# Kernel optimization log

Hardware: AMD Instinct MI355X
Metric: run time of the kernel (lower is better)

The kernel has to match this reference:

```python
import jax, jax.numpy as jnp
import numpy as np

# Static problem dims (match input_specs / init_kwargs)
B, NQ, C, H = 2, 900, 256, 8
HGT, WID = 64, 64            # single-scale feature map (input_spatial_shapes = [[64, 64]])
N = HGT * WID                # 4096 keys
DH = C // H                  # head dim 32
RPE_HID = 512
STRIDE = 16                  # feature_stride


def setup_inputs() -> dict:
    key = jax.random.key(0)
    ks = jax.random.split(key, 24)
    p = lambda k, shape: jax.random.normal(k, shape, jnp.float32) * 0.02
    # reference boxes (cx, cy, w, h) in pixel coords of a 1024x1024 image
    ref = jax.random.uniform(ks[0], (B, NQ, 1, 4), jnp.float32)
    ref = jnp.concatenate([ref[..., :2] * (WID * STRIDE), ref[..., 2:] * 128.0], axis=-1)
    return {
        "vggt_features": jnp.zeros((1,), jnp.float32),  # unused by forward (kept for signature fidelity)
        "query": jax.random.normal(ks[1], (B, NQ, C), jnp.float32),
        "reference_2d": ref,
        "k_input_flatten": jax.random.normal(ks[2], (B, N, C), jnp.float32),
        "v_input_flatten": jax.random.normal(ks[3], (B, N, C), jnp.float32),
        "input_spatial_shapes": jnp.array([[HGT, WID]], jnp.int32),
        "input_padding_mask": jnp.zeros((B, N), jnp.bool_),
        # cpb_mlp1 (x) and cpb_mlp2 (y): Linear(2,512)+ReLU+Linear(512,H,no bias); stored as [in,out]
        "W1x": p(ks[4], (2, RPE_HID)), "b1x": jnp.zeros((RPE_HID,), jnp.float32), "W2x": p(ks[5], (RPE_HID, H)),
        "W1y": p(ks[6], (2, RPE_HID)), "b1y": jnp.zeros((RPE_HID,), jnp.float32), "W2y": p(ks[7], (RPE_HID, H)),
        "Wq": p(ks[8], (C, C)), "bq": jnp.zeros((C,), jnp.float32),
        "Wk": p(ks[9], (C, C)), "bk": jnp.zeros((C,), jnp.float32),
        "Wv": p(ks[10], (C, C)), "bv": jnp.zeros((C,), jnp.float32),
        "Wp": p(ks[11], (C, C)), "bp": jnp.zeros((C,), jnp.float32),
    }


def _mlp(d, W1, b1, W2):
    return jax.nn.relu(d @ W1 + b1) @ W2


def reference(vggt_features, query, reference_2d, k_input_flatten, v_input_flatten,
              input_spatial_shapes, input_padding_mask,
              W1x, b1x, W2x, W1y, b1y, W2y, Wq, bq, Wk, bk, Wv, bv, Wp, bp):
    h, w = HGT, WID  # static (input_spatial_shapes[0] == [HGT, WID])
    scale = DH ** -0.5
    # cxcywh -> xyxy: [B, NQ, 1, 4]
    xyxy = jnp.concatenate([reference_2d[..., :2] - reference_2d[..., 2:] / 2,
                            reference_2d[..., :2] + reference_2d[..., 2:] / 2], axis=-1)
    # pixel-center grid coords (linspace(0.5, w-0.5, w) * stride)
    pos_x = ((jnp.arange(w, dtype=jnp.float32) + 0.5) * STRIDE)[None, None, :, None]
    pos_y = ((jnp.arange(h, dtype=jnp.float32) + 0.5) * STRIDE)[None, None, :, None]
    delta_x = xyxy[..., 0::2] - pos_x  # [B, NQ, w, 2]  (x1, x2 rel. to columns)
    delta_y = xyxy[..., 1::2] - pos_y  # [B, NQ, h, 2]  (y1, y2 rel. to rows)
    rpe_x = _mlp(delta_x, W1x, b1x, W2x)  # [B, NQ, w, H]
    rpe_y = _mlp(delta_y, W1y, b1y, W2y)  # [B, NQ, h, H]
    # broadcast add over (row, col) then flatten spatial -> [B, H, NQ, N]
    rpe = (rpe_x[:, :, None] + rpe_y[:, :, :, None]).reshape(B, NQ, h * w, H).transpose(0, 3, 1, 2)
    q = (query @ Wq + bq).reshape(B, NQ, H, DH).transpose(0, 2, 1, 3) * scale  # [B,H,NQ,DH]
    k = (k_input_flatten @ Wk + bk).reshape(B, N, H, DH).transpose(0, 2, 1, 3)  # [B,H,N,DH]
    v = (v_input_flatten @ Wv + bv).reshape(B, N, H, DH).transpose(0, 2, 1, 3)  # [B,H,N,DH]
    attn = jnp.einsum('bhqd,bhkd->bhqk', q, k) + rpe
    attn = attn + input_padding_mask[:, None, None, :].astype(attn.dtype) * (-100.0)
    # torch.clip_ to finfo(min,max) is an identity on finite values; softmax follows
    attn = jax.nn.softmax(attn, axis=-1)
    x = jnp.einsum('bhqk,bhkd->bhqd', attn, v).transpose(0, 2, 1, 3).reshape(B, NQ, C)
    return x @ Wp + bp
```

## Files before the change

kernel.cpp:

```cpp
#include <hip/hip_runtime.h>
#include <hip/hip_bf16.h>
#include <cmath>

#define B_ 2
#define NQ_ 900
#define N_ 4096
#define LOG2E 1.4426950408889634f

typedef __attribute__((ext_vector_type(4))) float f32x4;
typedef __attribute__((ext_vector_type(8))) short s16x8;
typedef __attribute__((ext_vector_type(8))) _Float16 f16x8;

__device__ inline short f2bf(float x) {
    union { __hip_bfloat16 b; short s; } u;
    u.b = __float2bfloat16(x);
    return u.s;
}
__device__ inline short f2h(float x) {
    _Float16 h = (_Float16)x;
    return __builtin_bit_cast(short, h);
}

template <int CTRL>
__device__ inline float dppf(float x) {
    int xi = __builtin_bit_cast(int, x);
    int r = __builtin_amdgcn_update_dpp(xi, xi, CTRL, 0xF, 0xF, true);
    return __builtin_bit_cast(float, r);
}
__device__ inline float rowmax16(float v) {
    v = fmaxf(v, dppf<0x121>(v));
    v = fmaxf(v, dppf<0x122>(v));
    v = fmaxf(v, dppf<0x124>(v));
    v = fmaxf(v, dppf<0x128>(v));
    return v;
}
__device__ inline float rowsum16(float v) {
    v += dppf<0x121>(v);
    v += dppf<0x122>(v);
    v += dppf<0x124>(v);
    v += dppf<0x128>(v);
    return v;
}

__global__ __launch_bounds__(256) void proj_kernel(
    const float* __restrict__ query, const float* __restrict__ kin,
    const float* __restrict__ vin,
    const float* __restrict__ Wq, const float* __restrict__ Wk,
    const float* __restrict__ Wv,
    const float* __restrict__ bqv, const float* __restrict__ bkv,
    const float* __restrict__ bvv,
    unsigned short* __restrict__ qbf, unsigned short* __restrict__ kbf,
    unsigned short* __restrict__ vbf, float qscale)
{
    const int mtx = blockIdx.z;
    const float* X = mtx == 0 ? query : mtx == 1 ? kin : vin;
    const float* W = mtx == 0 ? Wq : mtx == 1 ? Wk : Wv;
    const float* bias = mtx == 0 ? bqv : mtx == 1 ? bkv : bvv;
    unsigned short* Y = mtx == 0 ? qbf : mtx == 1 ? kbf : vbf;
    const int M = mtx == 0 ? 1800 : 8192;
    const int m0 = blockIdx.x * 64;
    if (m0 >= M) return;
    const float alpha = mtx == 0 ? qscale : 1.0f;
    const int rows_per_b = mtx == 0 ? 900 : 4096;
    const int ROWS = mtx == 0 ? 960 : 4096;

    __shared__ short Ab[16384];
    __shared__ short Bb[16384];
    const int tid = threadIdx.x;
    const int w = tid >> 6, l = tid & 63, quad = l >> 4, l15 = l & 15;
    const int wq = tid & 3, mm = tid >> 2;

    {
        const bool valid = (m0 + mm) < M;
        const float* xr = X + (size_t)(m0 + mm) * 256;
        #pragma unroll
        for (int it = 0; it < 8; ++it) {
            int g2 = it * 4 + wq;
            float4 a0 = make_float4(0.f, 0.f, 0.f, 0.f), a1 = a0;
            if (valid) {
                a0 = *(const float4*)(xr + g2 * 8);
                a1 = *(const float4*)(xr + g2 * 8 + 4);
            }
            uint4 pk;
            pk.x = (unsigned)(unsigned short)f2bf(a0.x) | ((unsigned)(unsigned short)f2bf(a0.y) << 16);
            pk.y = (unsigned)(unsigned short)f2bf(a0.z) | ((unsigned)(unsigned short)f2bf(a0.w) << 16);
            pk.z = (unsigned)(unsigned short)f2bf(a1.x) | ((unsigned)(unsigned short)f2bf(a1.y) << 16);
            pk.w = (unsigned)(unsigned short)f2bf(a1.z) | ((unsigned)(unsigned short)f2bf(a1.w) << 16);
            *(uint4*)(Ab + (it * 256 + mm * 4 + wq) * 8) = pk;
        }
    }

    for (int nt0 = 0; nt0 < 4; ++nt0) {
        const int n0 = nt0 * 64;
        {
            const float* wcol = W + n0 + mm;
            #pragma unroll
            for (int it = 0; it < 8; ++it) {
                int g2 = it * 4 + wq;
                uint4 wk4;
                wk4.x = (unsigned)(unsigned short)f2bf(wcol[(g2 * 8 + 0) * 256])
                      | ((unsigned)(unsigned short)f2bf(wcol[(g2 * 8 + 1) * 256]) << 16);
                wk4.y = (unsigned)(unsigned short)f2bf(wcol[(g2 * 8 + 2) * 256])
                      | ((unsigned)(unsigned short)f2bf(wcol[(g2 * 8 + 3) * 256]) << 16);
                wk4.z = (unsigned)(unsigned short)f2bf(wcol[(g2 * 8 + 4) * 256])
                      | ((unsigned)(unsigned short)f2bf(wcol[(g2 * 8 + 5) * 256]) << 16);
                wk4.w = (unsigned)(unsigned short)f2bf(wcol[(g2 * 8 + 6) * 256])
                      | ((unsigned)(unsigned short)f2bf(wcol[(g2 * 8 + 7) * 256]) << 16);
                *(uint4*)(Bb + (it * 256 + mm * 4 + wq) * 8) = wk4;
            }
        }
        __syncthreads();

        f32x4 acc[4] = {{0.f,0.f,0.f,0.f},{0.f,0.f,0.f,0.f},{0.f,0.f,0.f,0.f},{0.f,0.f,0.f,0.f}};
        #pragma unroll
        for (int kc = 0; kc < 8; ++kc) {
            s16x8 a = *(const s16x8*)(Ab + (kc * 256 + (w * 16 + l15) * 4 + quad) * 8);
            #pragma unroll
            for (int nt = 0; nt < 4; ++nt) {
                s16x8 bf = *(const s16x8*)(Bb + (kc * 256 + (nt * 16 + l15) * 4 + quad) * 8);
                acc[nt] = __builtin_amdgcn_mfma_f32_16x16x32_bf16(a, bf, acc[nt], 0, 0, 0);
            }
        }
        __syncthreads();

        #pragma unroll
        for (int nt = 0; nt < 4; ++nt) {
            int n = n0 + nt * 16 + l15;
            float bs = bias[n];
            int h = n >> 5, d = n & 31;
            #pragma unroll
            for (int r = 0; r < 4; ++r) {
                int row = m0 + w * 16 + quad * 4 + r;
                if (row < M) {
                    int b = row / rows_per_b;
                    int pos = row - b * rows_per_b;
                    Y[((size_t)(b * 8 + h) * ROWS + pos) * 32 + d] =
                        (unsigned short)f2bf((acc[nt][r] + bs) * alpha);
                }
            }
        }
    }
}

__global__ __launch_bounds__(256) void outproj_kernel(
    const float* __restrict__ X, const float* __restrict__ W,
    const float* __restrict__ bias, float* __restrict__ Y, int M)
{
    __shared__ short Abh[4096], Abl[4096], Bbh[4096], Bbl[4096];
    const int tid = threadIdx.x;
    const int m0 = blockIdx.x * 64, n0 = blockIdx.y * 64;
    const int w = tid >> 6, l = tid & 63, quad = l >> 4, l15 = l & 15;
    const int wq = tid & 3, mm = tid >> 2;
    const bool valid = (m0 + mm) < M;
    const float* xr = X + (size_t)(m0 + mm) * 256;
    const float* wcol = W + n0 + mm;

    f32x4 acc[4] = {{0.f,0.f,0.f,0.f},{0.f,0.f,0.f,0.f},{0.f,0.f,0.f,0.f},{0.f,0.f,0.f,0.f}};

    for (int kq = 0; kq < 4; ++kq) {
        #pragma unroll
        for (int it = 0; it < 2; ++it) {
            int g2 = it * 4 + wq;
            int kbase = kq * 64 + g2 * 8;
            float av[8], bv[8];
            #pragma unroll
            for (int j = 0; j < 8; ++j) {
                av[j] = valid ? xr[kbase + j] : 0.f;
                bv[j] = wcol[(kbase + j) * 256];
            }
            uint4 ah, al, bh, bl;
            unsigned* ahp = (unsigned*)&ah; unsigned* alp = (unsigned*)&al;
            unsigned* bhp = (unsigned*)&bh; unsigned* blp = (unsigned*)&bl;
            #pragma unroll
            for (int j2 = 0; j2 < 4; ++j2) {
                _Float16 h0 = (_Float16)av[j2 * 2], h1 = (_Float16)av[j2 * 2 + 1];
                ahp[j2] = (unsigned)(unsigned short)__builtin_bit_cast(short, h0)
                        | ((unsigned)(unsigned short)__builtin_bit_cast(short, h1) << 16);
                alp[j2] = (unsigned)(unsigned short)f2h(av[j2 * 2] - (float)h0)
                        | ((unsigned)(unsigned short)f2h(av[j2 * 2 + 1] - (float)h1) << 16);
                _Float16 g0 = (_Float16)bv[j2 * 2], g1 = (_Float16)bv[j2 * 2 + 1];
                bhp[j2] = (unsigned)(unsigned short)__builtin_bit_cast(short, g0)
                        | ((unsigned)(unsigned short)__builtin_bit_cast(short, g1) << 16);
                blp[j2] = (unsigned)(unsigned short)f2h(bv[j2 * 2] - (float)g0)
                        | ((unsigned)(unsigned short)f2h(bv[j2 * 2 + 1] - (float)g1) << 16);
            }
            int gi = (it * 256 + mm * 4 + wq) * 8;
            *(uint4*)(Abh + gi) = ah;
            *(uint4*)(Abl + gi) = al;
            *(uint4*)(Bbh + gi) = bh;
            *(uint4*)(Bbl + gi) = bl;
        }
        __syncthreads();

        #pragma unroll
        for (int kc = 0; kc < 2; ++kc) {
            int ga = (kc * 256 + (w * 16 + l15) * 4 + quad) * 8;
            f16x8 ah = *(const f16x8*)(Abh + ga);
            f16x8 al = *(const f16x8*)(Abl + ga);
            #pragma unroll
            for (int nt = 0; nt < 4; ++nt) {
                int gb = (kc * 256 + (nt * 16 + l15) * 4 + quad) * 8;
                f16x8 bh = *(const f16x8*)(Bbh + gb);
                f16x8 bl = *(const f16x8*)(Bbl + gb);
                acc[nt] = __builtin_amdgcn_mfma_f32_16x16x32_f16(ah, bh, acc[nt], 0, 0, 0);
                acc[nt] = __builtin_amdgcn_mfma_f32_16x16x32_f16(ah, bl, acc[nt], 0, 0, 0);
                acc[nt] = __builtin_amdgcn_mfma_f32_16x16x32_f16(al, bh, acc[nt], 0, 0, 0);
            }
        }
        __syncthreads();
    }

    #pragma unroll
    for (int nt = 0; nt < 4; ++nt) {
        int n = n0 + nt * 16 + l15;
        float bs = bias[n];
        #pragma unroll
        for (int r = 0; r < 4; ++r) {
            int row = m0 + w * 16 + quad * 4 + r;
            if (row < M)
                Y[(size_t)row * 256 + n] = acc[nt][r] + bs;
        }
    }
}

__global__ __launch_bounds__(512) void rpe3_kernel(
    const float* __restrict__ ref2d,
    const float* __restrict__ W1x, const float* __restrict__ b1x,
    const float* __restrict__ W1y, const float* __restrict__ b1y,
    const float* __restrict__ W2x, const float* __restrict__ W2y,
    float* __restrict__ rpe_x, float* __restrict__ rpe_y)
{
    __shared__ short sw2h[8192], sw2l[8192];
    __shared__ float4 sUV[2 * 576];

    const int tid = threadIdx.x;
    for (int i = tid; i < 8192; i += 512) {
        int g = i >> 3, j = i & 7;
        int kcg = g >> 6, rr = g & 63, n = rr >> 2, q4 = rr & 3;
        int k = kcg * 32 + q4 * 8 + j;
        float val = ((n < 8) ? W2x[k * 8 + n] : W2y[k * 8 + (n - 8)]) * LOG2E;
        _Float16 hi = (_Float16)val;
        sw2h[i] = __builtin_bit_cast(short, hi);
        sw2l[i] = f2h(val - (float)hi);
    }
    {
        int k = tid;
        float w1x0 = W1x[k], w1x1 = W1x[512 + k];
        float w1y0 = W1y[k], w1y1 = W1y[512 + k];
        float bx = b1x[k], by = b1y[k];
        float vx = -(w1x0 + w1x1), vy = -(w1y0 + w1y1);
        #pragma unroll
        for (int q2 = 0; q2 < 2; ++q2) {
            const float4 bb = *(const float4*)(ref2d + (size_t)(blockIdx.x * 2 + q2) * 4);
            float ux = fmaf(w1x0, bb.x - bb.z * 0.5f, fmaf(w1x1, bb.x + bb.z * 0.5f, bx));
            float uy = fmaf(w1y0, bb.y - bb.w * 0.5f, fmaf(w1y1, bb.y + bb.w * 0.5f, by));
            sUV[q2 * 576 + (k >> 3) * 9 + (k & 7)] = make_float4(ux, vx, uy, vy);
        }
    }

    const int w = tid >> 6, l = tid & 63, quad = l >> 4, l15 = l & 15;
    const int qi = w >> 2, wrow = w & 3;
    const int bq = blockIdx.x * 2 + qi;
    const int row = wrow * 16 + l15;
    const float pc = (row + 0.5f) * 16.0f;

    __syncthreads();

    f32x4 accx = {0.f, 0.f, 0.f, 0.f}, accy = {0.f, 0.f, 0.f, 0.f};
    for (int kc = 0; kc < 16; ++kc) {
        f16x8 axh, axl, ayh, ayl;
        #pragma unroll
        for (int i = 0; i < 8; ++i) {
            float4 u = sUV[qi * 576 + (kc * 4 + quad) * 9 + i];
            float hx = fmaxf(fmaf(u.y, pc, u.x), 0.f);
            float hy = fmaxf(fmaf(u.w, pc, u.z), 0.f);
            _Float16 xh = (_Float16)hx;
            _Float16 yh = (_Float16)hy;
            axh[i] = xh;
            axl[i] = (_Float16)(hx - (float)xh);
            ayh[i] = yh;
            ayl[i] = (_Float16)(hy - (float)yh);
        }
        f16x8 bh = *(const f16x8*)(sw2h + (kc * 64 + l15 * 4 + quad) * 8);
        f16x8 bl = *(const f16x8*)(sw2l + (kc * 64 + l15 * 4 + quad) * 8);
        accx = __builtin_amdgcn_mfma_f32_16x16x32_f16(axh, bh, accx, 0, 0, 0);
        accx = __builtin_amdgcn_mfma_f32_16x16x32_f16(axh, bl, accx, 0, 0, 0);
        accx = __builtin_amdgcn_mfma_f32_16x16x32_f16(axl, bh, accx, 0, 0, 0);
        accy = __builtin_amdgcn_mfma_f32_16x16x32_f16(ayh, bh, accy, 0, 0, 0);
        accy = __builtin_amdgcn_mfma_f32_16x16x32_f16(ayh, bl, accy, 0, 0, 0);
        accy = __builtin_amdgcn_mfma_f32_16x16x32_f16(ayl, bh, accy, 0, 0, 0);
    }

    #pragma unroll
    for (int rr = 0; rr < 4; ++rr) {
        int row_out = wrow * 16 + quad * 4 + rr;
        if (l15 < 8) rpe_x[((size_t)l15 * 1800 + bq) * 64 + row_out] = accx[rr];
        else         rpe_y[((size_t)(l15 - 8) * 1800 + bq) * 64 + row_out] = accy[rr];
    }
}

__global__ __launch_bounds__(512, 4) void attn_mfma_kernel(
    const unsigned short* __restrict__ qb16, const unsigned short* __restrict__ kb16,
    const unsigned short* __restrict__ vb16,
    const float* __restrict__ rpe_x, const float* __restrict__ rpe_y,
    const unsigned char* __restrict__ mask, float* __restrict__ xout)
{
    __shared__ short skf[4 * 2048];
    __shared__ short svt[4 * 2048];
    __shared__ short spb[8 * 544];
    __shared__ float ry[32 * 65];
    __shared__ unsigned long long smaskb[64];
    __shared__ float sm[8][16], sl[8][16], sLf[32];

    const int tid = threadIdx.x;
    const int qb = blockIdx.x, h = blockIdx.y, b = blockIdx.z;
    const int q0 = qb * 32;
    const int w = tid >> 6, l = tid & 63;
    const int qsub = w >> 2, g = w & 3;
    const int quad = l >> 4, l15 = l & 15;

    const unsigned short* qg = qb16 + (size_t)(b * 8 + h) * 960 * 32;
    const unsigned short* kg = kb16 + (size_t)(b * 8 + h) * 4096 * 32;
    const unsigned short* vg = vb16 + (size_t)(b * 8 + h) * 4096 * 32;
    const float* rxh = rpe_x + ((size_t)h * 1800 + b * NQ_) * 64;
    const float* ryh = rpe_y + ((size_t)h * 1800 + b * NQ_) * 64;

    for (int i = tid; i < 2048; i += 512) {
        int qq = q0 + (i >> 6), pos = i & 63;
        float vy = 0.f;
        if (qq < NQ_)
            vy = ryh[(size_t)qq * 64 + pos];
        ry[(i >> 6) * 65 + pos] = vy;
    }
    #pragma unroll
    for (int j = 0; j < 8; ++j) {
        int c = w * 8 + j;
        unsigned long long bits = __ballot(mask[(size_t)b * N_ + c * 64 + l] != 0);
        if (l == 0) smaskb[c] = bits;
    }

    s16x8 qa = *(const s16x8*)(qg + (size_t)(q0 + qsub * 16 + l15) * 32 + quad * 8);

    f32x4 rx4[4];
    #pragma unroll
    for (int t = 0; t < 4; ++t)
        #pragma unroll
        for (int r = 0; r < 4; ++r) {
            int qq = q0 + qsub * 16 + quad * 4 + r;
            rx4[t][r] = (qq < NQ_) ? rxh[(size_t)qq * 64 + t * 16 + l15] : 0.f;
        }

    const int sg = tid >> 7, role = (tid >> 6) & 1, stl = tid & 63;
    int eoff[4];
    if (role == 0) {
        #pragma unroll
        for (int t = 0; t < 4; ++t)
            eoff[t] = (t * 16 + (stl & 15)) * 32 + (stl >> 4) * 8;
    } else {
        #pragma unroll
        for (int t = 0; t < 4; ++t)
            eoff[t] = stl * 32 + t * 8;
    }
    const unsigned short* src = role ? vg : kg;

    uint4 pf[4];
    {
        size_t cb = (size_t)(sg * 16) * 2048;
        #pragma unroll
        for (int t = 0; t < 4; ++t) pf[t] = *(const uint4*)(src + cb + eoff[t]);
    }

    float mrow[4] = {-INFINITY, -INFINITY, -INFINITY, -INFINITY};
    float lrow[4] = {0.f, 0.f, 0.f, 0.f};
    f32x4 acc0 = {0.f, 0.f, 0.f, 0.f}, acc1 = {0.f, 0.f, 0.f, 0.f};
    short* pw = spb + w * 544;

    for (int i = 0; i < 16; ++i) {
        __syncthreads();
        if (role == 0) {
            #pragma unroll
            for (int t = 0; t < 4; ++t)
                *(uint4*)(skf + sg * 2048 + (t * 64 + stl) * 8) = pf[t];
        } else {
            short* vtw = svt + sg * 2048;
            #pragma unroll
            for (int t = 0; t < 4; ++t) {
                const unsigned short* pv = (const unsigned short*)&pf[t];
                #pragma unroll
                for (int j = 0; j < 8; ++j) {
                    int d = t * 8 + j;
                    vtw[d * 64 + (((stl >> 3) ^ (d & 7)) << 3) + (stl & 7)] = (short)pv[j];
                }
            }
        }
        __syncthreads();

        {
            int inext = (i + 1 < 16) ? i + 1 : 15;
            size_t cb = (size_t)(sg * 16 + inext) * 2048;
            #pragma unroll
            for (int t = 0; t < 4; ++t) pf[t] = *(const uint4*)(src + cb + eoff[t]);
        }

        const int cgc = g * 16 + i;
        const short* kf = skf + g * 2048;

        f32x4 sc[4];
        #pragma unroll
        for (int t = 0; t < 4; ++t) {
            s16x8 kb = *(const s16x8*)(kf + (t * 64 + l) * 8);
            sc[t] = __builtin_amdgcn_mfma_f32_16x16x32_bf16(qa, kb, rx4[t], 0, 0, 0);
        }
        float ryv[4];
        #pragma unroll
        for (int r = 0; r < 4; ++r)
            ryv[r] = ry[(qsub * 16 + quad * 4 + r) * 65 + cgc];
        unsigned long long mb = smaskb[cgc];
        if (mb) {
            #pragma unroll
            for (int t = 0; t < 4; ++t) {
                float mk = ((mb >> (t * 16 + l15)) & 1ULL) ? -144.2695f : 0.f;
                #pragma unroll
                for (int r = 0; r < 4; ++r) sc[t][r] += mk;
            }
        }

        float cmr[4];
        #pragma unroll
        for (int r = 0; r < 4; ++r)
            cmr[r] = fmaxf(fmaxf(sc[0][r], sc[1][r]), fmaxf(sc[2][r], sc[3][r])) + ryv[r];

        int ok = (cmr[0] <= mrow[0] + 8.f) & (cmr[1] <= mrow[1] + 8.f)
               & (cmr[2] <= mrow[2] + 8.f) & (cmr[3] <= mrow[3] + 8.f);
        if (!__all(ok)) {
            #pragma unroll
            for (int r = 0; r < 4; ++r) {
                float cm = rowmax16(cmr[r]);
                float mnew = fmaxf(mrow[r], cm);
                float al = exp2f(mrow[r] - mnew);
                mrow[r] = mnew;
                lrow[r] *= al;
                acc0[r] *= al;
                acc1[r] *= al;
            }
        }

        float msub[4];
        #pragma unroll
        for (int r = 0; r < 4; ++r) msub[r] = mrow[r] - ryv[r];
        #pragma unroll
        for (int t = 0; t < 4; ++t)
            #pragma unroll
            for (int r = 0; r < 4; ++r)
                sc[t][r] = exp2f(sc[t][r] - msub[r]);
        #pragma unroll
        for (int r = 0; r < 4; ++r)
            lrow[r] += (sc[0][r] + sc[1][r]) + (sc[2][r] + sc[3][r]);

        const short* vt = svt + g * 2048;
        #pragma unroll
        for (int hh = 0; hh < 2; ++hh) {
            #pragma unroll
            for (int tt = 0; tt < 2; ++tt) {
                int t = hh * 2 + tt;
                int gphys = (tt * 2 + (l15 >> 3)) ^ quad;
                #pragma unroll
                for (int r = 0; r < 4; ++r)
                    pw[(gphys * 17 + quad * 4 + r) * 8 + (l15 & 7)] = f2bf(sc[t][r]);
            }
            int gph_r = quad ^ (l15 >> 2);
            s16x8 pa  = *(const s16x8*)(pw + (gph_r * 17 + l15) * 8);
            int ksw = ((hh * 4 + quad) ^ (l15 & 7)) * 8;
            s16x8 vb0 = *(const s16x8*)(vt + l15 * 64 + ksw);
            s16x8 vb1 = *(const s16x8*)(vt + (16 + l15) * 64 + ksw);
            acc0 = __builtin_amdgcn_mfma_f32_16x16x32_bf16(pa, vb0, acc0, 0, 0, 0);
            acc1 = __builtin_amdgcn_mfma_f32_16x16x32_bf16(pa, vb1, acc1, 0, 0, 0);
        }
    }

    #pragma unroll
    for (int r = 0; r < 4; ++r) lrow[r] = rowsum16(lrow[r]);

    __syncthreads();
    if (l15 == 0) {
        #pragma unroll
        for (int r = 0; r < 4; ++r) {
            sm[w][quad * 4 + r] = mrow[r];
            sl[w][quad * 4 + r] = lrow[r];
        }
    }
    __syncthreads();
    float wgt[4], L4[4];
    #pragma unroll
    for (int r = 0; r < 4; ++r) {
        int qrow = quad * 4 + r;
        float mm = -INFINITY;
        #pragma unroll
        for (int gg = 0; gg < 4; ++gg) mm = fmaxf(mm, sm[qsub * 4 + gg][qrow]);
        float LL = 0.f;
        #pragma unroll
        for (int gg = 0; gg < 4; ++gg)
            LL += exp2f(sm[qsub * 4 + gg][qrow] - mm) * sl[qsub * 4 + gg][qrow];
        wgt[r] = exp2f(mrow[r] - mm);
        L4[r] = LL;
    }
    if (g == 0 && l15 == 0) {
        #pragma unroll
        for (int r = 0; r < 4; ++r) sLf[qsub * 16 + quad * 4 + r] = L4[r];
    }

    float* obuf = (float*)skf;
    for (int gg = 0; gg < 4; ++gg) {
        if (g == gg) {
            #pragma unroll
            for (int r = 0; r < 4; ++r) {
                int idx = (qsub * 16 + quad * 4 + r) * 33 + l15;
                float v0 = wgt[r] * acc0[r];
                float v1 = wgt[r] * acc1[r];
                if (gg == 0) { obuf[idx] = v0; obuf[idx + 16] = v1; }
                else         { obuf[idx] += v0; obuf[idx + 16] += v1; }
            }
        }
        __syncthreads();
    }

    for (int i = tid; i < 1024; i += 512) {
        int ql = i >> 5, d = i & 31;
        int qq = q0 + ql;
        if (qq < NQ_)
            xout[(size_t)(b * NQ_ + qq) * 256 + h * 32 + d] = obuf[ql * 33 + d] / sLf[ql];
    }
}

extern "C" void kernel_launch(void* const* d_in, const int* in_sizes, int n_in,
                              void* d_out, int out_size, void* d_ws, size_t ws_size,
                              hipStream_t stream)
{
    const float* query = (const float*)d_in[1];
    const float* ref2d = (const float*)d_in[2];
    const float* kin   = (const float*)d_in[3];
    const float* vin   = (const float*)d_in[4];
    const unsigned char* mask = (const unsigned char*)d_in[6];
    const float* W1x = (const float*)d_in[7];
    const float* b1x = (const float*)d_in[8];
    const float* W2x = (const float*)d_in[9];
    const float* W1y = (const float*)d_in[10];
    const float* b1y = (const float*)d_in[11];
    const float* W2y = (const float*)d_in[12];
    const float* Wq  = (const float*)d_in[13];
    const float* bq  = (const float*)d_in[14];
    const float* Wk  = (const float*)d_in[15];
    const float* bk  = (const float*)d_in[16];
    const float* Wv  = (const float*)d_in[17];
    const float* bv  = (const float*)d_in[18];
    const float* Wp  = (const float*)d_in[19];
    const float* bp  = (const float*)d_in[20];

    char* wsb = (char*)d_ws;
    unsigned short* qbf = (unsigned short*)(wsb);
    unsigned short* kbf = (unsigned short*)(wsb +   983040);
    unsigned short* vbf = (unsigned short*)(wsb +  5177344);
    float* rxws = (float*)(wsb +  9371648);
    float* ryws = (float*)(wsb + 13058048);
    float* xws  = (float*)(wsb + 16744448);
    float* out  = (float*)d_out;

    const float qscale = LOG2E / sqrtf(32.0f);

    proj_kernel<<<dim3(128, 1, 3), 256, 0, stream>>>(
        query, kin, vin, Wq, Wk, Wv, bq, bk, bv, qbf, kbf, vbf, qscale);
    rpe3_kernel<<<900, 512, 0, stream>>>(
        ref2d, W1x, b1x, W1y, b1y, W2x, W2y, rxws, ryws);
    attn_mfma_kernel<<<dim3(29, 8, B_), 512, 0, stream>>>(
        qbf, kbf, vbf, rxws, ryws, mask, xws);
    outproj_kernel<<<dim3(29, 4), 256, 0, stream>>>(xws, Wp, bp, out, 1800);
}
```

Before: 232.6 us.

## Split attention keys across two blocks and merge partial softmax results

Splits the 4096 keys into two halves handled by separate workgroups (split-K flash-decoding style), doubling the attention grid from 464 to 928 blocks so more of the GPU's compute units stay busy. Each block writes unnormalized partial outputs plus row max and sum to workspace. A new merge kernel rescales and combines the two partials into the final per-head output. This adds an extra kernel launch and extra workspace traffic in exchange for better occupancy.

```diff
diff --git a/kernel.cpp b/kernel.cpp
--- a/kernel.cpp
+++ b/kernel.cpp
@@ -303,50 +303,52 @@
     const unsigned short* __restrict__ qb16, const unsigned short* __restrict__ kb16,
     const unsigned short* __restrict__ vb16,
     const float* __restrict__ rpe_x, const float* __restrict__ rpe_y,
-    const unsigned char* __restrict__ mask, float* __restrict__ xout)
+    const unsigned char* __restrict__ mask, float* __restrict__ part)
 {
     __shared__ short skf[4 * 2048];
     __shared__ short svt[4 * 2048];
     __shared__ short spb[8 * 544];
-    __shared__ float ry[32 * 65];
-    __shared__ unsigned long long smaskb[64];
-    __shared__ float sm[8][16], sl[8][16], sLf[32];
+    __shared__ float sry[32 * 33];
+    __shared__ unsigned long long smaskb[32];
+    __shared__ float sm[8][16], sl[8][16], sMf[32], sLf[32];
 
     const int tid = threadIdx.x;
-    const int qb = blockIdx.x, h = blockIdx.y, b = blockIdx.z;
+    const int qb = blockIdx.x, b = blockIdx.z;
+    const int h = blockIdx.y & 7, kv = blockIdx.y >> 3;
     const int q0 = qb * 32;
     const int w = tid >> 6, l = tid & 63;
-    const int qsub = w >> 2, g = w & 3;
+    const int qsub = w >> 3 ? 0 : 0;
+    const int qs = w >> 2, g = w & 3;
     const int quad = l >> 4, l15 = l & 15;
 
     const unsigned short* qg = qb16 + (size_t)(b * 8 + h) * 960 * 32;
-    const unsigned short* kg = kb16 + (size_t)(b * 8 + h) * 4096 * 32;
-    const unsigned short* vg = vb16 + (size_t)(b * 8 + h) * 4096 * 32;
+    const unsigned short* kg = kb16 + (size_t)(b * 8 + h) * 4096 * 32 + (size_t)kv * 2048 * 32;
+    const unsigned short* vg = vb16 + (size_t)(b * 8 + h) * 4096 * 32 + (size_t)kv * 2048 * 32;
     const float* rxh = rpe_x + ((size_t)h * 1800 + b * NQ_) * 64;
     const float* ryh = rpe_y + ((size_t)h * 1800 + b * NQ_) * 64;
 
-    for (int i = tid; i < 2048; i += 512) {
-        int qq = q0 + (i >> 6), pos = i & 63;
+    for (int i = tid; i < 1024; i += 512) {
+        int qq = q0 + (i >> 5), p = i & 31;
         float vy = 0.f;
         if (qq < NQ_)
-            vy = ryh[(size_t)qq * 64 + pos];
-        ry[(i >> 6) * 65 + pos] = vy;
+            vy = ryh[(size_t)qq * 64 + kv * 32 + p];
+        sry[(i >> 5) * 33 + p] = vy;
     }
     #pragma unroll
-    for (int j = 0; j < 8; ++j) {
-        int c = w * 8 + j;
-        unsigned long long bits = __ballot(mask[(size_t)b * N_ + c * 64 + l] != 0);
+    for (int j = 0; j < 4; ++j) {
+        int c = w * 4 + j;
+        unsigned long long bits = __ballot(mask[(size_t)b * N_ + (kv * 32 + c) * 64 + l] != 0);
         if (l == 0) smaskb[c] = bits;
     }
 
-    s16x8 qa = *(const s16x8*)(qg + (size_t)(q0 + qsub * 16 + l15) * 32 + quad * 8);
+    s16x8 qa = *(const s16x8*)(qg + (size_t)(q0 + qs * 16 + l15) * 32 + quad * 8);
 
     f32x4 rx4[4];
     #pragma unroll
     for (int t = 0; t < 4; ++t)
         #pragma unroll
         for (int r = 0; r < 4; ++r) {
-            int qq = q0 + qsub * 16 + quad * 4 + r;
+            int qq = q0 + qs * 16 + quad * 4 + r;
             rx4[t][r] = (qq < NQ_) ? rxh[(size_t)qq * 64 + t * 16 + l15] : 0.f;
         }
 
@@ -365,7 +367,7 @@
 
     uint4 pf[4];
     {
-        size_t cb = (size_t)(sg * 16) * 2048;
+        size_t cb = (size_t)(sg * 8) * 2048;
         #pragma unroll
         for (int t = 0; t < 4; ++t) pf[t] = *(const uint4*)(src + cb + eoff[t]);
     }
@@ -375,7 +377,7 @@
     f32x4 acc0 = {0.f, 0.f, 0.f, 0.f}, acc1 = {0.f, 0.f, 0.f, 0.f};
     short* pw = spb + w * 544;
 
-    for (int i = 0; i < 16; ++i) {
+    for (int i = 0; i < 8; ++i) {
         __syncthreads();
         if (role == 0) {
             #pragma unroll
@@ -396,13 +398,13 @@
         __syncthreads();
 
         {
-            int inext = (i + 1 < 16) ? i + 1 : 15;
-            size_t cb = (size_t)(sg * 16 + inext) * 2048;
+            int inext = (i + 1 < 8) ? i + 1 : 7;
+            size_t cb = (size_t)(sg * 8 + inext) * 2048;
             #pragma unroll
             for (int t = 0; t < 4; ++t) pf[t] = *(const uint4*)(src + cb + eoff[t]);
         }
 
-        const int cgc = g * 16 + i;
+        const int lc = g * 8 + i;
         const short* kf = skf + g * 2048;
 
         f32x4 sc[4];
@@ -414,8 +416,8 @@
         float ryv[4];
         #pragma unroll
         for (int r = 0; r < 4; ++r)
-            ryv[r] = ry[(qsub * 16 + quad * 4 + r) * 65 + cgc];
-        unsigned long long mb = smaskb[cgc];
+            ryv[r] = sry[(qs * 16 + quad * 4 + r) * 33 + lc];
+        unsigned long long mb = smaskb[lc];
         if (mb) {
             #pragma unroll
             for (int t = 0; t < 4; ++t) {
@@ -490,23 +492,27 @@
         }
     }
     __syncthreads();
-    float wgt[4], L4[4];
+    float wgt[4], L4[4], M4[4];
     #pragma unroll
     for (int r = 0; r < 4; ++r) {
         int qrow = quad * 4 + r;
         float mm = -INFINITY;
         #pragma unroll
-        for (int gg = 0; gg < 4; ++gg) mm = fmaxf(mm, sm[qsub * 4 + gg][qrow]);
+        for (int gg = 0; gg < 4; ++gg) mm = fmaxf(mm, sm[qs * 4 + gg][qrow]);
         float LL = 0.f;
         #pragma unroll
         for (int gg = 0; gg < 4; ++gg)
-            LL += exp2f(sm[qsub * 4 + gg][qrow] - mm) * sl[qsub * 4 + gg][qrow];
+            LL += exp2f(sm[qs * 4 + gg][qrow] - mm) * sl[qs * 4 + gg][qrow];
         wgt[r] = exp2f(mrow[r] - mm);
         L4[r] = LL;
+        M4[r] = mm;
     }
     if (g == 0 && l15 == 0) {
         #pragma unroll
-        for (int r = 0; r < 4; ++r) sLf[qsub * 16 + quad * 4 + r] = L4[r];
+        for (int r = 0; r < 4; ++r) {
+            sLf[qs * 16 + quad * 4 + r] = L4[r];
+            sMf[qs * 16 + quad * 4 + r] = M4[r];
+        }
     }
 
     float* obuf = (float*)skf;
@@ -514,7 +520,7 @@
         if (g == gg) {
             #pragma unroll
             for (int r = 0; r < 4; ++r) {
-                int idx = (qsub * 16 + quad * 4 + r) * 33 + l15;
+                int idx = (qs * 16 + quad * 4 + r) * 33 + l15;
                 float v0 = wgt[r] * acc0[r];
                 float v1 = wgt[r] * acc1[r];
                 if (gg == 0) { obuf[idx] = v0; obuf[idx + 16] = v1; }
@@ -524,11 +530,43 @@
         __syncthreads();
     }
 
-    for (int i = tid; i < 1024; i += 512) {
-        int ql = i >> 5, d = i & 31;
-        int qq = q0 + ql;
-        if (qq < NQ_)
-            xout[(size_t)(b * NQ_ + qq) * 256 + h * 32 + d] = obuf[ql * 33 + d] / sLf[ql];
+    float* po = part + (size_t)(((b * 8 + h) * 29 + qb) * 2 + kv) * 1088;
+    for (int i = tid; i < 1024; i += 512)
+        po[i] = obuf[(i >> 5) * 33 + (i & 31)];
+    if (tid < 32) {
+        po[1024 + tid] = sMf[tid];
+        po[1056 + tid] = sLf[tid];
+    }
+}
+
+__global__ __launch_bounds__(256) void attn_merge_kernel(
+    const float* __restrict__ part, float* __restrict__ xout)
+{
+    const int qb = blockIdx.x, h = blockIdx.y, b = blockIdx.z;
+    const float* p0 = part + (size_t)(((b * 8 + h) * 29 + qb) * 2) * 1088;
+    const float* p1 = p0 + 1088;
+    __shared__ float a0s[32], a1s[32], iLs[32];
+    const int tid = threadIdx.x;
+    if (tid < 32) {
+        float m0 = p0[1024 + tid], m1 = p1[1024 + tid];
+        float M = fmaxf(m0, m1);
+        float a0 = exp2f(m0 - M), a1 = exp2f(m1 - M);
+        float L = a0 * p0[1056 + tid] + a1 * p1[1056 + tid];
+        a0s[tid] = a0; a1s[tid] = a1; iLs[tid] = 1.0f / L;
+    }
+    __syncthreads();
+    int i = tid * 4;
+    int ql = i >> 5, d = i & 31;
+    int qq = qb * 32 + ql;
+    if (qq < NQ_) {
+        const f32x4 v0 = *(const f32x4*)(p0 + i);
+        const f32x4 v1 = *(const f32x4*)(p1 + i);
+        float a0 = a0s[ql], a1 = a1s[ql], iL = iLs[ql];
+        f32x4 o;
+        #pragma unroll
+        for (int j = 0; j < 4; ++j)
+            o[j] = (a0 * v0[j] + a1 * v1[j]) * iL;
+        *(f32x4*)(&xout[(size_t)(b * NQ_ + qq) * 256 + h * 32 + d]) = o;
     }
 }
 
@@ -563,6 +601,7 @@
     float* rxws = (float*)(wsb +  9371648);
     float* ryws = (float*)(wsb + 13058048);
     float* xws  = (float*)(wsb + 16744448);
+    float* part = (float*)(wsb + 18587648);
     float* out  = (float*)d_out;
 
     const float qscale = LOG2E / sqrtf(32.0f);
@@ -571,7 +610,8 @@
         query, kin, vin, Wq, Wk, Wv, bq, bk, bv, qbf, kbf, vbf, qscale);
     rpe3_kernel<<<900, 512, 0, stream>>>(
         ref2d, W1x, b1x, W1y, b1y, W2x, W2y, rxws, ryws);
-    attn_mfma_kernel<<<dim3(29, 8, B_), 512, 0, stream>>>(
-        qbf, kbf, vbf, rxws, ryws, mask, xws);
+    attn_mfma_kernel<<<dim3(29, 16, B_), 512, 0, stream>>>(
+        qbf, kbf, vbf, rxws, ryws, mask, part);
+    attn_merge_kernel<<<dim3(29, 8, B_), 256, 0, stream>>>(part, xws);
     outproj_kernel<<<dim3(29, 4), 256, 0, stream>>>(xws, Wp, bp, out, 1800);
 }
```

New measurement: 235.0 us. No clear change (+1.0%).

## Pre-convert and transpose weights once in a prep kernel, read B operands from global

Applied to the files above, without the earlier changes.

Adds a prep kernel that converts Wq/Wk/Wv to bf16, Wp to fp16 hi/lo pairs, and W2x/W2y to scaled fp16 hi/lo, all in transposed layouts. The projection, output-projection and RPE kernels then load B operands directly from global or L2 instead of each block redoing strided fp32 loads and conversions into shared memory. This removes redundant per-block weight conversion and shared memory use. It adds a kernel launch, and the MFMA loops now wait on global loads rather than LDS reads.

```diff
diff --git a/kernel.cpp b/kernel.cpp
--- a/kernel.cpp
+++ b/kernel.cpp
@@ -42,11 +42,75 @@
     return v;
 }
 
+__global__ __launch_bounds__(256) void prep_kernel(
+    const float* __restrict__ Wq, const float* __restrict__ Wk,
+    const float* __restrict__ Wv, const float* __restrict__ Wp,
+    const float* __restrict__ W2x, const float* __restrict__ W2y,
+    unsigned short* __restrict__ wtq, unsigned short* __restrict__ wtk,
+    unsigned short* __restrict__ wtv, unsigned short* __restrict__ wph,
+    unsigned short* __restrict__ wpl, unsigned short* __restrict__ w2h,
+    unsigned short* __restrict__ w2l)
+{
+    const int bx = blockIdx.x;
+    const int tid = threadIdx.x;
+    if (bx == 64) {
+        for (int i = tid; i < 8192; i += 256) {
+            int g = i >> 3, j = i & 7;
+            int kcg = g >> 6, rr = g & 63, n = rr >> 2, q4 = rr & 3;
+            int k = kcg * 32 + q4 * 8 + j;
+            float val = ((n < 8) ? W2x[k * 8 + n] : W2y[k * 8 + (n - 8)]) * LOG2E;
+            _Float16 hi = (_Float16)val;
+            w2h[i] = (unsigned short)__builtin_bit_cast(short, hi);
+            w2l[i] = (unsigned short)f2h(val - (float)hi);
+        }
+        return;
+    }
+    const int mtx = bx >> 4, tile = bx & 15;
+    const int kt = tile >> 2, ntile = tile & 3;
+    const float* W = mtx == 0 ? Wq : mtx == 1 ? Wk : mtx == 2 ? Wv : Wp;
+    __shared__ unsigned short th[64][72];
+    __shared__ unsigned short tl[64][72];
+    #pragma unroll
+    for (int p = 0; p < 4; ++p) {
+        int kl = p * 16 + (tid >> 4);
+        int nl = (tid & 15) * 4;
+        float4 v = *(const float4*)(W + (size_t)(kt * 64 + kl) * 256 + ntile * 64 + nl);
+        float vv[4] = {v.x, v.y, v.z, v.w};
+        #pragma unroll
+        for (int i = 0; i < 4; ++i) {
+            if (mtx < 3) {
+                th[nl + i][kl] = (unsigned short)f2bf(vv[i]);
+            } else {
+                _Float16 h = (_Float16)vv[i];
+                th[nl + i][kl] = (unsigned short)__builtin_bit_cast(short, h);
+                tl[nl + i][kl] = (unsigned short)f2h(vv[i] - (float)h);
+            }
+        }
+    }
+    __syncthreads();
+    unsigned short* dst = mtx == 0 ? wtq : mtx == 1 ? wtk : mtx == 2 ? wtv : wph;
+    #pragma unroll
+    for (int p = 0; p < 2; ++p) {
+        int nl = p * 32 + (tid >> 3);
+        int k8 = (tid & 7) * 8;
+        uint4 pk;
+        unsigned short* ps = (unsigned short*)&pk;
+        #pragma unroll
+        for (int j = 0; j < 8; ++j) ps[j] = th[nl][k8 + j];
+        *(uint4*)(dst + (size_t)(ntile * 64 + nl) * 256 + kt * 64 + k8) = pk;
+        if (mtx == 3) {
+            #pragma unroll
+            for (int j = 0; j < 8; ++j) ps[j] = tl[nl][k8 + j];
+            *(uint4*)(wpl + (size_t)(ntile * 64 + nl) * 256 + kt * 64 + k8) = pk;
+        }
+    }
+}
+
 __global__ __launch_bounds__(256) void proj_kernel(
     const float* __restrict__ query, const float* __restrict__ kin,
     const float* __restrict__ vin,
-    const float* __restrict__ Wq, const float* __restrict__ Wk,
-    const float* __restrict__ Wv,
+    const unsigned short* __restrict__ wtq, const unsigned short* __restrict__ wtk,
+    const unsigned short* __restrict__ wtv,
     const float* __restrict__ bqv, const float* __restrict__ bkv,
     const float* __restrict__ bvv,
     unsigned short* __restrict__ qbf, unsigned short* __restrict__ kbf,
@@ -54,7 +118,7 @@
 {
     const int mtx = blockIdx.z;
     const float* X = mtx == 0 ? query : mtx == 1 ? kin : vin;
-    const float* W = mtx == 0 ? Wq : mtx == 1 ? Wk : Wv;
+    const unsigned short* WT = mtx == 0 ? wtq : mtx == 1 ? wtk : wtv;
     const float* bias = mtx == 0 ? bqv : mtx == 1 ? bkv : bvv;
     unsigned short* Y = mtx == 0 ? qbf : mtx == 1 ? kbf : vbf;
     const int M = mtx == 0 ? 1800 : 8192;
@@ -65,7 +129,6 @@
     const int ROWS = mtx == 0 ? 960 : 4096;
 
     __shared__ short Ab[16384];
-    __shared__ short Bb[16384];
     const int tid = threadIdx.x;
     const int w = tid >> 6, l = tid & 63, quad = l >> 4, l15 = l & 15;
     const int wq = tid & 3, mm = tid >> 2;
@@ -89,39 +152,20 @@
             *(uint4*)(Ab + (it * 256 + mm * 4 + wq) * 8) = pk;
         }
     }
+    __syncthreads();
 
     for (int nt0 = 0; nt0 < 4; ++nt0) {
         const int n0 = nt0 * 64;
-        {
-            const float* wcol = W + n0 + mm;
-            #pragma unroll
-            for (int it = 0; it < 8; ++it) {
-                int g2 = it * 4 + wq;
-                uint4 wk4;
-                wk4.x = (unsigned)(unsigned short)f2bf(wcol[(g2 * 8 + 0) * 256])
-                      | ((unsigned)(unsigned short)f2bf(wcol[(g2 * 8 + 1) * 256]) << 16);
-                wk4.y = (unsigned)(unsigned short)f2bf(wcol[(g2 * 8 + 2) * 256])
-                      | ((unsigned)(unsigned short)f2bf(wcol[(g2 * 8 + 3) * 256]) << 16);
-                wk4.z = (unsigned)(unsigned short)f2bf(wcol[(g2 * 8 + 4) * 256])
-                      | ((unsigned)(unsigned short)f2bf(wcol[(g2 * 8 + 5) * 256]) << 16);
-                wk4.w = (unsigned)(unsigned short)f2bf(wcol[(g2 * 8 + 6) * 256])
-                      | ((unsigned)(unsigned short)f2bf(wcol[(g2 * 8 + 7) * 256]) << 16);
-                *(uint4*)(Bb + (it * 256 + mm * 4 + wq) * 8) = wk4;
-            }
-        }
-        __syncthreads();
-
         f32x4 acc[4] = {{0.f,0.f,0.f,0.f},{0.f,0.f,0.f,0.f},{0.f,0.f,0.f,0.f},{0.f,0.f,0.f,0.f}};
         #pragma unroll
         for (int kc = 0; kc < 8; ++kc) {
             s16x8 a = *(const s16x8*)(Ab + (kc * 256 + (w * 16 + l15) * 4 + quad) * 8);
             #pragma unroll
             for (int nt = 0; nt < 4; ++nt) {
-                s16x8 bf = *(const s16x8*)(Bb + (kc * 256 + (nt * 16 + l15) * 4 + quad) * 8);
+                s16x8 bf = *(const s16x8*)(WT + (size_t)(n0 + nt * 16 + l15) * 256 + kc * 32 + quad * 8);
                 acc[nt] = __builtin_amdgcn_mfma_f32_16x16x32_bf16(a, bf, acc[nt], 0, 0, 0);
             }
         }
-        __syncthreads();
 
         #pragma unroll
         for (int nt = 0; nt < 4; ++nt) {
@@ -143,17 +187,17 @@
 }
 
 __global__ __launch_bounds__(256) void outproj_kernel(
-    const float* __restrict__ X, const float* __restrict__ W,
+    const float* __restrict__ X,
+    const unsigned short* __restrict__ wph, const unsigned short* __restrict__ wpl,
     const float* __restrict__ bias, float* __restrict__ Y, int M)
 {
-    __shared__ short Abh[4096], Abl[4096], Bbh[4096], Bbl[4096];
+    __shared__ short Abh[4096], Abl[4096];
     const int tid = threadIdx.x;
     const int m0 = blockIdx.x * 64, n0 = blockIdx.y * 64;
     const int w = tid >> 6, l = tid & 63, quad = l >> 4, l15 = l & 15;
     const int wq = tid & 3, mm = tid >> 2;
     const bool valid = (m0 + mm) < M;
     const float* xr = X + (size_t)(m0 + mm) * 256;
-    const float* wcol = W + n0 + mm;
 
     f32x4 acc[4] = {{0.f,0.f,0.f,0.f},{0.f,0.f,0.f,0.f},{0.f,0.f,0.f,0.f},{0.f,0.f,0.f,0.f}};
 
@@ -162,15 +206,12 @@
         for (int it = 0; it < 2; ++it) {
             int g2 = it * 4 + wq;
             int kbase = kq * 64 + g2 * 8;
-            float av[8], bv[8];
-            #pragma unroll
-            for (int j = 0; j < 8; ++j) {
+            float av[8];
+            #pragma unroll
+            for (int j = 0; j < 8; ++j)
                 av[j] = valid ? xr[kbase + j] : 0.f;
-                bv[j] = wcol[(kbase + j) * 256];
-            }
-            uint4 ah, al, bh, bl;
+            uint4 ah, al;
             unsigned* ahp = (unsigned*)&ah; unsigned* alp = (unsigned*)&al;
-            unsigned* bhp = (unsigned*)&bh; unsigned* blp = (unsigned*)&bl;
             #pragma unroll
             for (int j2 = 0; j2 < 4; ++j2) {
                 _Float16 h0 = (_Float16)av[j2 * 2], h1 = (_Float16)av[j2 * 2 + 1];
@@ -178,17 +219,10 @@
                         | ((unsigned)(unsigned short)__builtin_bit_cast(short, h1) << 16);
                 alp[j2] = (unsigned)(unsigned short)f2h(av[j2 * 2] - (float)h0)
                         | ((unsigned)(unsigned short)f2h(av[j2 * 2 + 1] - (float)h1) << 16);
-                _Float16 g0 = (_Float16)bv[j2 * 2], g1 = (_Float16)bv[j2 * 2 + 1];
-                bhp[j2] = (unsigned)(unsigned short)__builtin_bit_cast(short, g0)
-                        | ((unsigned)(unsigned short)__builtin_bit_cast(short, g1) << 16);
-                blp[j2] = (unsigned)(unsigned short)f2h(bv[j2 * 2] - (float)g0)
-                        | ((unsigned)(unsigned short)f2h(bv[j2 * 2 + 1] - (float)g1) << 16);
             }
             int gi = (it * 256 + mm * 4 + wq) * 8;
             *(uint4*)(Abh + gi) = ah;
             *(uint4*)(Abl + gi) = al;
-            *(uint4*)(Bbh + gi) = bh;
-            *(uint4*)(Bbl + gi) = bl;
         }
         __syncthreads();
 
@@ -199,9 +233,9 @@
             f16x8 al = *(const f16x8*)(Abl + ga);
             #pragma unroll
             for (int nt = 0; nt < 4; ++nt) {
-                int gb = (kc * 256 + (nt * 16 + l15) * 4 + quad) * 8;
-                f16x8 bh = *(const f16x8*)(Bbh + gb);
-                f16x8 bl = *(const f16x8*)(Bbl + gb);
+                size_t gb = (size_t)(n0 + nt * 16 + l15) * 256 + kq * 64 + kc * 32 + quad * 8;
+                f16x8 bh = *(const f16x8*)(wph + gb);
+                f16x8 bl = *(const f16x8*)(wpl + gb);
                 acc[nt] = __builtin_amdgcn_mfma_f32_16x16x32_f16(ah, bh, acc[nt], 0, 0, 0);
                 acc[nt] = __builtin_amdgcn_mfma_f32_16x16x32_f16(ah, bl, acc[nt], 0, 0, 0);
                 acc[nt] = __builtin_amdgcn_mfma_f32_16x16x32_f16(al, bh, acc[nt], 0, 0, 0);
@@ -227,22 +261,12 @@
     const float* __restrict__ ref2d,
     const float* __restrict__ W1x, const float* __restrict__ b1x,
     const float* __restrict__ W1y, const float* __restrict__ b1y,
-    const float* __restrict__ W2x, const float* __restrict__ W2y,
+    const unsigned short* __restrict__ w2h, const unsigned short* __restrict__ w2l,
     float* __restrict__ rpe_x, float* __restrict__ rpe_y)
 {
-    __shared__ short sw2h[8192], sw2l[8192];
     __shared__ float4 sUV[2 * 576];
 
     const int tid = threadIdx.x;
-    for (int i = tid; i < 8192; i += 512) {
-        int g = i >> 3, j = i & 7;
-        int kcg = g >> 6, rr = g & 63, n = rr >> 2, q4 = rr & 3;
-        int k = kcg * 32 + q4 * 8 + j;
-        float val = ((n < 8) ? W2x[k * 8 + n] : W2y[k * 8 + (n - 8)]) * LOG2E;
-        _Float16 hi = (_Float16)val;
-        sw2h[i] = __builtin_bit_cast(short, hi);
-        sw2l[i] = f2h(val - (float)hi);
-    }
     {
         int k = tid;
         float w1x0 = W1x[k], w1x1 = W1x[512 + k];
@@ -281,8 +305,8 @@
             ayh[i] = yh;
             ayl[i] = (_Float16)(hy - (float)yh);
         }
-        f16x8 bh = *(const f16x8*)(sw2h + (kc * 64 + l15 * 4 + quad) * 8);
-        f16x8 bl = *(const f16x8*)(sw2l + (kc * 64 + l15 * 4 + quad) * 8);
+        f16x8 bh = *(const f16x8*)(w2h + (kc * 64 + l15 * 4 + quad) * 8);
+        f16x8 bl = *(const f16x8*)(w2l + (kc * 64 + l15 * 4 + quad) * 8);
         accx = __builtin_amdgcn_mfma_f32_16x16x32_f16(axh, bh, accx, 0, 0, 0);
         accx = __builtin_amdgcn_mfma_f32_16x16x32_f16(axh, bl, accx, 0, 0, 0);
         accx = __builtin_amdgcn_mfma_f32_16x16x32_f16(axl, bh, accx, 0, 0, 0);
@@ -563,15 +587,24 @@
     float* rxws = (float*)(wsb +  9371648);
     float* ryws = (float*)(wsb + 13058048);
     float* xws  = (float*)(wsb + 16744448);
+    unsigned short* wtq = (unsigned short*)(wsb + 18587648);
+    unsigned short* wtk = (unsigned short*)(wsb + 18718720);
+    unsigned short* wtv = (unsigned short*)(wsb + 18849792);
+    unsigned short* wph = (unsigned short*)(wsb + 18980864);
+    unsigned short* wpl = (unsigned short*)(wsb + 19111936);
+    unsigned short* w2h = (unsigned short*)(wsb + 19243008);
+    unsigned short* w2l = (unsigned short*)(wsb + 19259392);
     float* out  = (float*)d_out;
 
     const float qscale = LOG2E / sqrtf(32.0f);
 
+    prep_kernel<<<65, 256, 0, stream>>>(
+        Wq, Wk, Wv, Wp, W2x, W2y, wtq, wtk, wtv, wph, wpl, w2h, w2l);
     proj_kernel<<<dim3(128, 1, 3), 256, 0, stream>>>(
-        query, kin, vin, Wq, Wk, Wv, bq, bk, bv, qbf, kbf, vbf, qscale);
+        query, kin, vin, wtq, wtk, wtv, bq, bk, bv, qbf, kbf, vbf, qscale);
     rpe3_kernel<<<900, 512, 0, stream>>>(
-        ref2d, W1x, b1x, W1y, b1y, W2x, W2y, rxws, ryws);
+        ref2d, W1x, b1x, W1y, b1y, w2h, w2l, rxws, ryws);
     attn_mfma_kernel<<<dim3(29, 8, B_), 512, 0, stream>>>(
         qbf, kbf, vbf, rxws, ryws, mask, xws);
-    outproj_kernel<<<dim3(29, 4), 256, 0, stream>>>(xws, Wp, bp, out, 1800);
-}
+    outproj_kernel<<<dim3(29, 4), 256, 0, stream>>>(xws, wph, wpl, bp, out, 1800);
+}
```

Measured after the change: 243.2 us. 4.5% more time.
